# Kernel tuning notes

Hardware: AMD Instinct MI355X
Metric: run time of the kernel (lower is better)

## Reference

```python
import jax, jax.numpy as jnp
import numpy as np
import itertools

B, G, FEAT, IMG = 2048, 8, 512, 1024
SCALES = list(range(G, 1, -1))  # [8,7,6,5,4,3,2]
SUBSAMPLE = 12


def setup_inputs() -> dict:
    key = jax.random.key(0)
    keys = jax.random.split(key, 1 + 2 * len(SCALES))
    rng = np.random.default_rng(0)
    inp = {"input": jax.random.normal(keys[0], (B, G, FEAT), dtype=jnp.float32)}
    for i, scale in enumerate(SCALES):
        perms = np.array(list(itertools.permutations(range(G), scale)), dtype=np.int32)
        n_sub = min(SUBSAMPLE, len(perms))
        sel = rng.choice(len(perms), n_sub, replace=False)
        inp[f"perms{i}"] = jnp.asarray(perms[sel])  # [n_sub, scale] int32
        lim = 1.0 / np.sqrt(scale * FEAT)
        inp[f"W{i}"] = jax.random.uniform(keys[1 + 2 * i], (IMG, scale * FEAT), minval=-lim, maxval=lim, dtype=jnp.float32)
        inp[f"b{i}"] = jax.random.uniform(keys[2 + 2 * i], (IMG,), minval=-lim, maxval=lim, dtype=jnp.float32)
    return inp


def _forward(input, perms_list, W_list, b_list):
    outs = []
    for perms, W, b in zip(perms_list, W_list, b_list):
        # gather: [B, n_sub, scale, FEAT] -> [B, n_sub, scale*FEAT]
        g = input[:, perms, :]
        g = g.reshape(g.shape[0], g.shape[1], -1)
        # batched linear over all subsamples, then mean over subsamples
        y = jnp.einsum('bsf,df->bsd', g, W) + b  # [B, n_sub, IMG]
        outs.append(y.mean(axis=1))
    return jnp.concatenate(outs, axis=1)  # [B, len(SCALES)*IMG]


def reference(input, perms0, W0, b0, perms1, W1, b1, perms2, W2, b2,
              perms3, W3, b3, perms4, W4, b4, perms5, W5, b5, perms6, W6, b6):
    perms_list = [perms0, perms1, perms2, perms3, perms4, perms5, perms6]
    W_list = [W0, W1, W2, W3, W4, W5, W6]
    b_list = [b0, b1, b2, b3, b4, b5, b6]
    return _forward(input, perms_list, W_list, b_list)
```

## Files before the change

kernel.cpp:

```cpp
#include <hip/hip_runtime.h>

typedef unsigned short u16;
typedef __bf16 bf16x8 __attribute__((ext_vector_type(8)));
typedef float f32x4 __attribute__((ext_vector_type(4)));

__device__ __forceinline__ u16 f2bf(float f) {
  unsigned int u = __float_as_uint(f);
  return (u16)((u + 0x7fffu + ((u >> 16) & 1u)) >> 16);
}

__device__ __forceinline__ int cumK(int i) { return 256 * i * (17 - i); }

__global__ __launch_bounds__(256) void k_xbar(
    const float* __restrict__ x,
    const int* p0, const int* p1, const int* p2, const int* p3,
    const int* p4, const int* p5, const int* p6,
    u16* __restrict__ Xb) {
  __shared__ float sc[448];
  const int b = blockIdx.x;
  const int t = threadIdx.x;
  const int* ps[7] = {p0, p1, p2, p3, p4, p5, p6};
  for (int cell = t; cell < 448; cell += 256) {
    int i = cell >> 6, rem = cell & 63, g = rem >> 3, j = rem & 7;
    int scale = 8 - i;
    float v = 0.f;
    if (j < scale) {
      const int* p = ps[i];
      int cnt = 0;
      for (int s = 0; s < 12; ++s) cnt += (p[s * scale + j] == g) ? 1 : 0;
      v = (float)cnt * (1.0f / 12.0f);
    }
    sc[cell] = v;
  }
  __syncthreads();
  const int u = t & 63;
  const int wv = t >> 6;
  const float4* xrow = reinterpret_cast<const float4*>(x + (size_t)b * 4096);
  float4 xr0[8], xr1[8];
#pragma unroll
  for (int g = 0; g < 8; ++g) {
    xr0[g] = xrow[g * 128 + u * 2];
    xr1[g] = xrow[g * 128 + u * 2 + 1];
  }
  u16* orow = Xb + (size_t)b * 17920;
  for (int s = wv; s < 35; s += 4) {
    int i = 0, rem = s;
    while (rem >= 8 - i) { rem -= 8 - i; ++i; }
    const int j = rem;
    float4 A0 = make_float4(0.f, 0.f, 0.f, 0.f);
    float4 A1 = make_float4(0.f, 0.f, 0.f, 0.f);
#pragma unroll
    for (int g = 0; g < 8; ++g) {
      const float c = sc[i * 64 + g * 8 + j];
      A0.x += c * xr0[g].x; A0.y += c * xr0[g].y;
      A0.z += c * xr0[g].z; A0.w += c * xr0[g].w;
      A1.x += c * xr1[g].x; A1.y += c * xr1[g].y;
      A1.z += c * xr1[g].z; A1.w += c * xr1[g].w;
    }
    uint4 o;
    o.x = (unsigned)f2bf(A0.x) | ((unsigned)f2bf(A0.y) << 16);
    o.y = (unsigned)f2bf(A0.z) | ((unsigned)f2bf(A0.w) << 16);
    o.z = (unsigned)f2bf(A1.x) | ((unsigned)f2bf(A1.y) << 16);
    o.w = (unsigned)f2bf(A1.z) | ((unsigned)f2bf(A1.w) << 16);
    *reinterpret_cast<uint4*>(orow + cumK(i) + j * 512 + u * 8) = o;
  }
}

__global__ __launch_bounds__(256) void k_wcast(
    const float* W0, const float* W1, const float* W2, const float* W3,
    const float* W4, const float* W5, const float* W6,
    u16* __restrict__ Wcat) {
  int i = 0, rem = blockIdx.x;
  while (rem >= (8 - i) * 512) { rem -= (8 - i) * 512; ++i; }
  const float* Wi = (i == 0) ? W0 : (i == 1) ? W1 : (i == 2) ? W2 :
                    (i == 3) ? W3 : (i == 4) ? W4 : (i == 5) ? W5 : W6;
  const int t = threadIdx.x;
  const float4 w = reinterpret_cast<const float4*>(Wi)[(size_t)rem * 256 + t];
  ushort4 o;
  o.x = f2bf(w.x); o.y = f2bf(w.y); o.z = f2bf(w.z); o.w = f2bf(w.w);
  reinterpret_cast<ushort4*>(Wcat + ((size_t)cumK(i) + rem) * 1024)[t] = o;
}

__device__ __forceinline__ void gl_lds16(const u16* g, u16* l) {
  __builtin_amdgcn_global_load_lds(
      (const __attribute__((address_space(1))) void*)g,
      (__attribute__((address_space(3))) void*)l, 16, 0, 0);
}

#define WAIT_VM8 0x0F78
#define WAIT_VM0 0x0F70

__global__ __launch_bounds__(256) void k_gemm_ms(
    const u16* __restrict__ Xb, const u16* __restrict__ Wcat,
    const float* b0, const float* b1, const float* b2, const float* b3,
    const float* b4, const float* b5, const float* b6,
    float* __restrict__ out) {
  __shared__ u16 lds[2 * 16384];
  const int i = blockIdx.x >> 7;
  const int s = blockIdx.x & 127;
  const int region = s & 7;
  const int k = s >> 3;
  const int mq = region >> 1;
  const int nq = region & 1;
  const int m0 = (mq * 4 + (k & 3)) * 128;
  const int n0loc = (nq * 4 + (k >> 2)) * 128;
  const int K = (8 - i) * 512;
  const int niter = K >> 6;
  const size_t baseB = (size_t)cumK(i) * 1024;

  const int tid = threadIdx.x;
  const int lane = tid & 63;
  const int wave = tid >> 6;
  const int quad = lane >> 4;
  const int l15 = lane & 15;
  const int waveM = (wave >> 1) * 64;
  const int waveN = (wave & 1) * 64;

  const int srow = tid >> 3;
  const int sslot = tid & 7;
  const int gch = (sslot - srow) & 7;
  const u16* pA0 = Xb + (size_t)(m0 + srow) * 17920 + cumK(i) + gch * 8;
  const u16* pB0 = Wcat + baseB + (size_t)(n0loc + srow) * K + gch * 8;
  const size_t strideAj = (size_t)32 * 17920;
  const size_t strideBj = (size_t)32 * K;
  u16* lA0 = lds + tid * 8;
  u16* lB0 = lds + 8192 + tid * 8;

  int offA[2][4], offB[2][4];
#pragma unroll
  for (int t = 0; t < 2; ++t) {
#pragma unroll
    for (int q = 0; q < 4; ++q) {
      int rowA = waveM + q * 16 + l15;
      offA[t][q] = rowA * 64 + (((t * 4 + quad) + rowA) & 7) * 8;
      int rowB = waveN + q * 16 + l15;
      offB[t][q] = 8192 + rowB * 64 + (((t * 4 + quad) + rowB) & 7) * 8;
    }
  }

  f32x4 acc[4][4];
#pragma unroll
  for (int q = 0; q < 4; ++q)
#pragma unroll
    for (int c = 0; c < 4; ++c) {
      f32x4 z = {0.f, 0.f, 0.f, 0.f};
      acc[q][c] = z;
    }

#pragma unroll
  for (int j = 0; j < 4; ++j) {
    gl_lds16(pA0 + j * strideAj, lA0 + j * 2048);
    gl_lds16(pB0 + j * strideBj, lB0 + j * 2048);
  }

  for (int kt = 0; kt < niter - 1; ++kt) {
    const size_t ko = (size_t)(kt + 1) * 64;
    const int nb = ((kt + 1) & 1) << 14;
#pragma unroll
    for (int j = 0; j < 4; ++j) {
      gl_lds16(pA0 + j * strideAj + ko, lA0 + nb + j * 2048);
      gl_lds16(pB0 + j * strideBj + ko, lB0 + nb + j * 2048);
    }
    __builtin_amdgcn_s_waitcnt(WAIT_VM8);
    __builtin_amdgcn_s_barrier();
    const int boff = (kt & 1) << 14;
#pragma unroll
    for (int t = 0; t < 2; ++t) {
      bf16x8 av[4], bv[4];
#pragma unroll
      for (int q = 0; q < 4; ++q) av[q] = *reinterpret_cast<const bf16x8*>(lds + boff + offA[t][q]);
#pragma unroll
      for (int c = 0; c < 4; ++c) bv[c] = *reinterpret_cast<const bf16x8*>(lds + boff + offB[t][c]);
#pragma unroll
      for (int q = 0; q < 4; ++q)
#pragma unroll
        for (int c = 0; c < 4; ++c)
          acc[q][c] = __builtin_amdgcn_mfma_f32_16x16x32_bf16(av[q], bv[c], acc[q][c], 0, 0, 0);
    }
    __builtin_amdgcn_s_barrier();
  }

  __builtin_amdgcn_s_waitcnt(WAIT_VM0);
  __builtin_amdgcn_s_barrier();
  {
    const int boff = ((niter - 1) & 1) << 14;
#pragma unroll
    for (int t = 0; t < 2; ++t) {
      bf16x8 av[4], bv[4];
#pragma unroll
      for (int q = 0; q < 4; ++q) av[q] = *reinterpret_cast<const bf16x8*>(lds + boff + offA[t][q]);
#pragma unroll
      for (int c = 0; c < 4; ++c) bv[c] = *reinterpret_cast<const bf16x8*>(lds + boff + offB[t][c]);
#pragma unroll
      for (int q = 0; q < 4; ++q)
#pragma unroll
        for (int c = 0; c < 4; ++c)
          acc[q][c] = __builtin_amdgcn_mfma_f32_16x16x32_bf16(av[q], bv[c], acc[q][c], 0, 0, 0);
    }
  }

  const float* bi = (i == 0) ? b0 : (i == 1) ? b1 : (i == 2) ? b2 :
                    (i == 3) ? b3 : (i == 4) ? b4 : (i == 5) ? b5 : b6;
#pragma unroll
  for (int c = 0; c < 4; ++c) {
    const int nloc = n0loc + waveN + c * 16 + l15;
    const float bias = bi[nloc];
    const int ncol = i * 1024 + nloc;
#pragma unroll
    for (int q = 0; q < 4; ++q) {
      const int mbase = m0 + waveM + q * 16 + quad * 4;
#pragma unroll
      for (int reg = 0; reg < 4; ++reg)
        out[(size_t)(mbase + reg) * 7168 + ncol] = acc[q][c][reg] + bias;
    }
  }
}

extern "C" void kernel_launch(void* const* d_in, const int* in_sizes, int n_in,
                              void* d_out, int out_size, void* d_ws, size_t ws_size,
                              hipStream_t stream) {
  const float* input = (const float*)d_in[0];
  const int* perms[7];
  const float* W[7];
  const float* bias[7];
  for (int i = 0; i < 7; ++i) {
    perms[i] = (const int*)d_in[1 + 3 * i];
    W[i]     = (const float*)d_in[2 + 3 * i];
    bias[i]  = (const float*)d_in[3 + 3 * i];
  }
  char* ws = (char*)d_ws;
  u16* Xb   = (u16*)ws;
  u16* Wcat = (u16*)(ws + (size_t)2048 * 17920 * 2);

  k_xbar<<<2048, 256, 0, stream>>>(input, perms[0], perms[1], perms[2], perms[3],
                                   perms[4], perms[5], perms[6], Xb);
  k_wcast<<<17920, 256, 0, stream>>>(W[0], W[1], W[2], W[3], W[4], W[5], W[6], Wcat);
  k_gemm_ms<<<896, 256, 0, stream>>>(Xb, Wcat,
                                     bias[0], bias[1], bias[2], bias[3],
                                     bias[4], bias[5], bias[6],
                                     (float*)d_out);
}
```

Baseline: 283.1 us.

## Fold subsample count matrix into weights and run uniform K=4096 GEMM

Instead of building a per-scale mixed input of width 17920, the count matrix is folded into the weights, giving a transformed weight of shape 7168x4096. The input is simply cast to bf16. The GEMM then runs with a uniform K of 4096 across all output columns, with an XCD-aware tile mapping. This shrinks the intermediate activation buffer and balances tile work, but it raises the GEMM multiply-add count and adds a weight-mixing prep kernel that fuses the old cast and xbar kernels.

```diff
diff --git a/kernel.cpp b/kernel.cpp
--- a/kernel.cpp
+++ b/kernel.cpp
@@ -9,76 +9,87 @@
   return (u16)((u + 0x7fffu + ((u >> 16) & 1u)) >> 16);
 }
 
-__device__ __forceinline__ int cumK(int i) { return 256 * i * (17 - i); }
-
-__global__ __launch_bounds__(256) void k_xbar(
+
+__global__ __launch_bounds__(256) void k_prep(
     const float* __restrict__ x,
     const int* p0, const int* p1, const int* p2, const int* p3,
     const int* p4, const int* p5, const int* p6,
-    u16* __restrict__ Xb) {
-  __shared__ float sc[448];
-  const int b = blockIdx.x;
-  const int t = threadIdx.x;
-  const int* ps[7] = {p0, p1, p2, p3, p4, p5, p6};
-  for (int cell = t; cell < 448; cell += 256) {
-    int i = cell >> 6, rem = cell & 63, g = rem >> 3, j = rem & 7;
-    int scale = 8 - i;
-    float v = 0.f;
-    if (j < scale) {
-      const int* p = ps[i];
-      int cnt = 0;
-      for (int s = 0; s < 12; ++s) cnt += (p[s * scale + j] == g) ? 1 : 0;
-      v = (float)cnt * (1.0f / 12.0f);
-    }
-    sc[cell] = v;
-  }
-  __syncthreads();
-  const int u = t & 63;
-  const int wv = t >> 6;
-  const float4* xrow = reinterpret_cast<const float4*>(x + (size_t)b * 4096);
-  float4 xr0[8], xr1[8];
-#pragma unroll
-  for (int g = 0; g < 8; ++g) {
-    xr0[g] = xrow[g * 128 + u * 2];
-    xr1[g] = xrow[g * 128 + u * 2 + 1];
-  }
-  u16* orow = Xb + (size_t)b * 17920;
-  for (int s = wv; s < 35; s += 4) {
-    int i = 0, rem = s;
-    while (rem >= 8 - i) { rem -= 8 - i; ++i; }
-    const int j = rem;
-    float4 A0 = make_float4(0.f, 0.f, 0.f, 0.f);
-    float4 A1 = make_float4(0.f, 0.f, 0.f, 0.f);
-#pragma unroll
-    for (int g = 0; g < 8; ++g) {
-      const float c = sc[i * 64 + g * 8 + j];
-      A0.x += c * xr0[g].x; A0.y += c * xr0[g].y;
-      A0.z += c * xr0[g].z; A0.w += c * xr0[g].w;
-      A1.x += c * xr1[g].x; A1.y += c * xr1[g].y;
-      A1.z += c * xr1[g].z; A1.w += c * xr1[g].w;
-    }
-    uint4 o;
-    o.x = (unsigned)f2bf(A0.x) | ((unsigned)f2bf(A0.y) << 16);
-    o.y = (unsigned)f2bf(A0.z) | ((unsigned)f2bf(A0.w) << 16);
-    o.z = (unsigned)f2bf(A1.x) | ((unsigned)f2bf(A1.y) << 16);
-    o.w = (unsigned)f2bf(A1.z) | ((unsigned)f2bf(A1.w) << 16);
-    *reinterpret_cast<uint4*>(orow + cumK(i) + j * 512 + u * 8) = o;
-  }
-}
-
-__global__ __launch_bounds__(256) void k_wcast(
     const float* W0, const float* W1, const float* W2, const float* W3,
     const float* W4, const float* W5, const float* W6,
-    u16* __restrict__ Wcat) {
-  int i = 0, rem = blockIdx.x;
-  while (rem >= (8 - i) * 512) { rem -= (8 - i) * 512; ++i; }
-  const float* Wi = (i == 0) ? W0 : (i == 1) ? W1 : (i == 2) ? W2 :
-                    (i == 3) ? W3 : (i == 4) ? W4 : (i == 5) ? W5 : W6;
+    u16* __restrict__ Xb16, u16* __restrict__ Wtil) {
+  __shared__ float sC[64];
+  const int bid = blockIdx.x;
   const int t = threadIdx.x;
-  const float4 w = reinterpret_cast<const float4*>(Wi)[(size_t)rem * 256 + t];
-  ushort4 o;
-  o.x = f2bf(w.x); o.y = f2bf(w.y); o.z = f2bf(w.z); o.w = f2bf(w.w);
-  reinterpret_cast<ushort4*>(Wcat + ((size_t)cumK(i) + rem) * 1024)[t] = o;
+  if (bid < 1792) {
+    const int r0 = bid << 2;
+    const int i = r0 >> 10;
+    const int scale = 8 - i;
+    const int K = scale << 9;
+    const int d0 = r0 - (i << 10);
+    if (t < 64) {
+      const int g = t >> 3, j = t & 7;
+      float v = 0.f;
+      if (j < scale) {
+        const int* p = (i == 0) ? p0 : (i == 1) ? p1 : (i == 2) ? p2 :
+                       (i == 3) ? p3 : (i == 4) ? p4 : (i == 5) ? p5 : p6;
+        int cnt = 0;
+        for (int s = 0; s < 12; ++s) cnt += (p[s * scale + j] == g) ? 1 : 0;
+        v = (float)cnt * (1.0f / 12.0f);
+      }
+      sC[t] = v;
+    }
+    __syncthreads();
+    const float* Wi = (i == 0) ? W0 : (i == 1) ? W1 : (i == 2) ? W2 :
+                      (i == 3) ? W3 : (i == 4) ? W4 : (i == 5) ? W5 : W6;
+    const int u = t & 63;
+    const int gq = t >> 6;
+    u16* dst = Wtil + ((size_t)r0 << 12);
+    for (int r = 0; r < 4; ++r) {
+      const float* wrow = Wi + (size_t)(d0 + r) * K;
+      float a0[8], a1[8];
+#pragma unroll
+      for (int e = 0; e < 8; ++e) { a0[e] = 0.f; a1[e] = 0.f; }
+      for (int j = 0; j < scale; ++j) {
+        const float* wp = wrow + j * 512 + (u << 3);
+        const float4 wa = *reinterpret_cast<const float4*>(wp);
+        const float4 wb = *reinterpret_cast<const float4*>(wp + 4);
+        const float c0 = sC[(gq << 4) + j];
+        const float c1 = sC[(gq << 4) + 8 + j];
+        a0[0] += c0 * wa.x; a0[1] += c0 * wa.y; a0[2] += c0 * wa.z; a0[3] += c0 * wa.w;
+        a0[4] += c0 * wb.x; a0[5] += c0 * wb.y; a0[6] += c0 * wb.z; a0[7] += c0 * wb.w;
+        a1[0] += c1 * wa.x; a1[1] += c1 * wa.y; a1[2] += c1 * wa.z; a1[3] += c1 * wa.w;
+        a1[4] += c1 * wb.x; a1[5] += c1 * wb.y; a1[6] += c1 * wb.z; a1[7] += c1 * wb.w;
+      }
+      uint4 o0, o1;
+      o0.x = (unsigned)f2bf(a0[0]) | ((unsigned)f2bf(a0[1]) << 16);
+      o0.y = (unsigned)f2bf(a0[2]) | ((unsigned)f2bf(a0[3]) << 16);
+      o0.z = (unsigned)f2bf(a0[4]) | ((unsigned)f2bf(a0[5]) << 16);
+      o0.w = (unsigned)f2bf(a0[6]) | ((unsigned)f2bf(a0[7]) << 16);
+      o1.x = (unsigned)f2bf(a1[0]) | ((unsigned)f2bf(a1[1]) << 16);
+      o1.y = (unsigned)f2bf(a1[2]) | ((unsigned)f2bf(a1[3]) << 16);
+      o1.z = (unsigned)f2bf(a1[4]) | ((unsigned)f2bf(a1[5]) << 16);
+      o1.w = (unsigned)f2bf(a1[6]) | ((unsigned)f2bf(a1[7]) << 16);
+      u16* drow = dst + ((size_t)r << 12) + (gq << 10) + (u << 3);
+      *reinterpret_cast<uint4*>(drow) = o0;
+      *reinterpret_cast<uint4*>(drow + 512) = o1;
+    }
+  } else {
+    const int tid0 = ((bid - 1792) << 8) | t;
+    const float4* X4 = reinterpret_cast<const float4*>(x);
+    uint4* O = reinterpret_cast<uint4*>(Xb16);
+#pragma unroll 4
+    for (int it = 0; it < 16; ++it) {
+      const int e = tid0 + (it << 16);
+      const float4 a = X4[(size_t)e * 2];
+      const float4 c = X4[(size_t)e * 2 + 1];
+      uint4 o;
+      o.x = (unsigned)f2bf(a.x) | ((unsigned)f2bf(a.y) << 16);
+      o.y = (unsigned)f2bf(a.z) | ((unsigned)f2bf(a.w) << 16);
+      o.z = (unsigned)f2bf(c.x) | ((unsigned)f2bf(c.y) << 16);
+      o.w = (unsigned)f2bf(c.z) | ((unsigned)f2bf(c.w) << 16);
+      O[e] = o;
+    }
+  }
 }
 
 __device__ __forceinline__ void gl_lds16(const u16* g, u16* l) {
@@ -90,23 +101,17 @@
 #define WAIT_VM8 0x0F78
 #define WAIT_VM0 0x0F70
 
-__global__ __launch_bounds__(256) void k_gemm_ms(
-    const u16* __restrict__ Xb, const u16* __restrict__ Wcat,
+__global__ __launch_bounds__(256) void k_gemm(
+    const u16* __restrict__ A, const u16* __restrict__ Bm,
     const float* b0, const float* b1, const float* b2, const float* b3,
     const float* b4, const float* b5, const float* b6,
     float* __restrict__ out) {
   __shared__ u16 lds[2 * 16384];
-  const int i = blockIdx.x >> 7;
-  const int s = blockIdx.x & 127;
-  const int region = s & 7;
-  const int k = s >> 3;
-  const int mq = region >> 1;
-  const int nq = region & 1;
-  const int m0 = (mq * 4 + (k & 3)) * 128;
-  const int n0loc = (nq * 4 + (k >> 2)) * 128;
-  const int K = (8 - i) * 512;
-  const int niter = K >> 6;
-  const size_t baseB = (size_t)cumK(i) * 1024;
+  const int bid = blockIdx.x;
+  const int xcd = bid & 7;
+  const int sid = bid >> 3;
+  const int m0 = (sid & 15) * 128;
+  const int n0 = (xcd * 7 + (sid >> 4)) * 128;
 
   const int tid = threadIdx.x;
   const int lane = tid & 63;
@@ -119,22 +124,21 @@
   const int srow = tid >> 3;
   const int sslot = tid & 7;
   const int gch = (sslot - srow) & 7;
-  const u16* pA0 = Xb + (size_t)(m0 + srow) * 17920 + cumK(i) + gch * 8;
-  const u16* pB0 = Wcat + baseB + (size_t)(n0loc + srow) * K + gch * 8;
-  const size_t strideAj = (size_t)32 * 17920;
-  const size_t strideBj = (size_t)32 * K;
+  const u16* pA0 = A + (size_t)(m0 + srow) * 4096 + gch * 8;
+  const u16* pB0 = Bm + (size_t)(n0 + srow) * 4096 + gch * 8;
+  const size_t strideR = (size_t)32 * 4096;
   u16* lA0 = lds + tid * 8;
   u16* lB0 = lds + 8192 + tid * 8;
 
   int offA[2][4], offB[2][4];
 #pragma unroll
-  for (int t = 0; t < 2; ++t) {
+  for (int tt = 0; tt < 2; ++tt) {
 #pragma unroll
     for (int q = 0; q < 4; ++q) {
       int rowA = waveM + q * 16 + l15;
-      offA[t][q] = rowA * 64 + (((t * 4 + quad) + rowA) & 7) * 8;
+      offA[tt][q] = rowA * 64 + (((tt * 4 + quad) + rowA) & 7) * 8;
       int rowB = waveN + q * 16 + l15;
-      offB[t][q] = 8192 + rowB * 64 + (((t * 4 + quad) + rowB) & 7) * 8;
+      offB[tt][q] = 8192 + rowB * 64 + (((tt * 4 + quad) + rowB) & 7) * 8;
     }
   }
 
@@ -149,28 +153,28 @@
 
 #pragma unroll
   for (int j = 0; j < 4; ++j) {
-    gl_lds16(pA0 + j * strideAj, lA0 + j * 2048);
-    gl_lds16(pB0 + j * strideBj, lB0 + j * 2048);
-  }
-
-  for (int kt = 0; kt < niter - 1; ++kt) {
+    gl_lds16(pA0 + j * strideR, lA0 + j * 2048);
+    gl_lds16(pB0 + j * strideR, lB0 + j * 2048);
+  }
+
+  for (int kt = 0; kt < 63; ++kt) {
     const size_t ko = (size_t)(kt + 1) * 64;
     const int nb = ((kt + 1) & 1) << 14;
 #pragma unroll
     for (int j = 0; j < 4; ++j) {
-      gl_lds16(pA0 + j * strideAj + ko, lA0 + nb + j * 2048);
-      gl_lds16(pB0 + j * strideBj + ko, lB0 + nb + j * 2048);
+      gl_lds16(pA0 + j * strideR + ko, lA0 + nb + j * 2048);
+      gl_lds16(pB0 + j * strideR + ko, lB0 + nb + j * 2048);
     }
     __builtin_amdgcn_s_waitcnt(WAIT_VM8);
     __builtin_amdgcn_s_barrier();
     const int boff = (kt & 1) << 14;
 #pragma unroll
-    for (int t = 0; t < 2; ++t) {
+    for (int tt = 0; tt < 2; ++tt) {
       bf16x8 av[4], bv[4];
 #pragma unroll
-      for (int q = 0; q < 4; ++q) av[q] = *reinterpret_cast<const bf16x8*>(lds + boff + offA[t][q]);
-#pragma unroll
-      for (int c = 0; c < 4; ++c) bv[c] = *reinterpret_cast<const bf16x8*>(lds + boff + offB[t][c]);
+      for (int q = 0; q < 4; ++q) av[q] = *reinterpret_cast<const bf16x8*>(lds + boff + offA[tt][q]);
+#pragma unroll
+      for (int c = 0; c < 4; ++c) bv[c] = *reinterpret_cast<const bf16x8*>(lds + boff + offB[tt][c]);
 #pragma unroll
       for (int q = 0; q < 4; ++q)
 #pragma unroll
@@ -183,14 +187,14 @@
   __builtin_amdgcn_s_waitcnt(WAIT_VM0);
   __builtin_amdgcn_s_barrier();
   {
-    const int boff = ((niter - 1) & 1) << 14;
-#pragma unroll
-    for (int t = 0; t < 2; ++t) {
+    const int boff = 1 << 14;
+#pragma unroll
+    for (int tt = 0; tt < 2; ++tt) {
       bf16x8 av[4], bv[4];
 #pragma unroll
-      for (int q = 0; q < 4; ++q) av[q] = *reinterpret_cast<const bf16x8*>(lds + boff + offA[t][q]);
-#pragma unroll
-      for (int c = 0; c < 4; ++c) bv[c] = *reinterpret_cast<const bf16x8*>(lds + boff + offB[t][c]);
+      for (int q = 0; q < 4; ++q) av[q] = *reinterpret_cast<const bf16x8*>(lds + boff + offA[tt][q]);
+#pragma unroll
+      for (int c = 0; c < 4; ++c) bv[c] = *reinterpret_cast<const bf16x8*>(lds + boff + offB[tt][c]);
 #pragma unroll
       for (int q = 0; q < 4; ++q)
 #pragma unroll
@@ -199,13 +203,13 @@
     }
   }
 
-  const float* bi = (i == 0) ? b0 : (i == 1) ? b1 : (i == 2) ? b2 :
-                    (i == 3) ? b3 : (i == 4) ? b4 : (i == 5) ? b5 : b6;
+  const int isc = n0 >> 10;
+  const float* bi = (isc == 0) ? b0 : (isc == 1) ? b1 : (isc == 2) ? b2 :
+                    (isc == 3) ? b3 : (isc == 4) ? b4 : (isc == 5) ? b5 : b6;
 #pragma unroll
   for (int c = 0; c < 4; ++c) {
-    const int nloc = n0loc + waveN + c * 16 + l15;
-    const float bias = bi[nloc];
-    const int ncol = i * 1024 + nloc;
+    const int ncol = n0 + waveN + c * 16 + l15;
+    const float bias = bi[ncol & 1023];
 #pragma unroll
     for (int q = 0; q < 4; ++q) {
       const int mbase = m0 + waveM + q * 16 + quad * 4;
@@ -229,14 +233,16 @@
     bias[i]  = (const float*)d_in[3 + 3 * i];
   }
   char* ws = (char*)d_ws;
-  u16* Xb   = (u16*)ws;
-  u16* Wcat = (u16*)(ws + (size_t)2048 * 17920 * 2);
-
-  k_xbar<<<2048, 256, 0, stream>>>(input, perms[0], perms[1], perms[2], perms[3],
-                                   perms[4], perms[5], perms[6], Xb);
-  k_wcast<<<17920, 256, 0, stream>>>(W[0], W[1], W[2], W[3], W[4], W[5], W[6], Wcat);
-  k_gemm_ms<<<896, 256, 0, stream>>>(Xb, Wcat,
-                                     bias[0], bias[1], bias[2], bias[3],
-                                     bias[4], bias[5], bias[6],
-                                     (float*)d_out);
-}
+  u16* Xb16 = (u16*)ws;
+  u16* Wtil = (u16*)(ws + (size_t)2048 * 4096 * 2);
+
+  k_prep<<<2048, 256, 0, stream>>>(input,
+                                   perms[0], perms[1], perms[2], perms[3],
+                                   perms[4], perms[5], perms[6],
+                                   W[0], W[1], W[2], W[3], W[4], W[5], W[6],
+                                   Xb16, Wtil);
+  k_gemm<<<896, 256, 0, stream>>>(Xb16, Wtil,
+                                  bias[0], bias[1], bias[2], bias[3],
+                                  bias[4], bias[5], bias[6],
+                                  (float*)d_out);
+}
```

After: 325.7 us. 15.0% more time.
